# Performance work log

Hardware: AMD Instinct MI355X
Metric: run time of the kernel (lower is better)

Reference implementation:

```python
import jax, jax.numpy as jnp
import numpy as np

B, C, T, H = 16, 128, 128, 128


def setup_inputs() -> dict:
    key = jax.random.key(0)
    ks = jax.random.split(key, 9)
    inp = {
        "food_relation": jax.random.normal(ks[0], (B, C, H), jnp.float32),
        "thorn_relation": jax.random.normal(ks[1], (B, C, T, H), jnp.float32),
        "clone": jax.random.normal(ks[2], (B, C, H), jnp.float32),
        "clone_relation": jax.random.normal(ks[3], (B, C, C, H), jnp.float32),
        "thorn_mask": jax.random.randint(ks[4], (B, T), 0, 2, jnp.int32),
        "clone_mask": jax.random.randint(ks[5], (B, C), 0, 2, jnp.int32),
        # MLP(layer_num=1) == Linear(in, h) + activation (ReLU)
        "W_thorn": jax.random.normal(ks[6], (2 * H, H), jnp.float32) / np.sqrt(2 * H),
        "b_thorn": jnp.zeros((H,), jnp.float32),
        "W_clone": jax.random.normal(ks[7], (3 * H, H), jnp.float32) / np.sqrt(3 * H),
        "b_clone": jnp.zeros((H,), jnp.float32),
        "W_agg": jax.random.normal(ks[8], (4 * H, H), jnp.float32) / np.sqrt(4 * H),
        "b_agg": jnp.zeros((H,), jnp.float32),
    }
    return inp


def reference(food_relation, thorn_relation, clone, clone_relation,
              thorn_mask, clone_mask,
              W_thorn, b_thorn, W_clone, b_clone, W_agg, b_agg):
    b, c, h = clone.shape
    t = thorn_relation.shape[2]
    tm = thorn_mask.astype(clone.dtype)[:, None, :, None]  # (b,1,t,1)
    cm = clone_mask.astype(clone.dtype)[:, None, :, None]  # (b,1,c,1)

    # thorn branch: MLP(concat([clone_i, thorn_rel_ij], -1))
    # == clone @ W[:h] (broadcast over t) + rel @ W[h:], avoiding the big concat
    x = ((clone @ W_thorn[:h])[:, :, None, :]
         + jnp.einsum('bcth,hk->bctk', thorn_relation, W_thorn[h:])
         + b_thorn)  # (b,c,t,h)
    thorn_agg = jnp.max(jax.nn.relu(x) * tm, axis=2)  # (b,c,h)

    # clone branch: MLP(concat([clone_i, clone_j, clone_rel_ij], -1))
    y = ((clone @ W_clone[:h])[:, :, None, :]
         + (clone @ W_clone[h:2 * h])[:, None, :, :]
         + jnp.einsum('bcdh,hk->bcdk', clone_relation, W_clone[2 * h:])
         + b_clone)  # (b,c,c,h)
    clone_agg = jnp.max(jax.nn.relu(y) * cm, axis=2)  # (b,c,h)

    agg = jnp.concatenate([clone, food_relation, thorn_agg, clone_agg], axis=-1)  # (b,c,4h)
    return clone + jax.nn.relu(agg @ W_agg + b_agg)
```

## Files before the change

kernel.cpp:

```cpp
#include <hip/hip_runtime.h>

#define BB 16
#define CC 128
#define TT 128
#define HH 128
#define BC (BB*CC)

typedef __attribute__((ext_vector_type(8))) short bf16x8;
typedef __attribute__((ext_vector_type(4))) float f32x4;

__device__ __forceinline__ unsigned short f2bf(float f) {
  union { float f; unsigned u; } v; v.f = f;
  unsigned u = v.u;
  u += 0x7FFFu + ((u >> 16) & 1u);
  return (unsigned short)(u >> 16);
}

__device__ __forceinline__ bf16x8 pack8(f32x4 a, f32x4 b) {
  bf16x8 r;
  r[0] = (short)f2bf(a[0]); r[1] = (short)f2bf(a[1]);
  r[2] = (short)f2bf(a[2]); r[3] = (short)f2bf(a[3]);
  r[4] = (short)f2bf(b[0]); r[5] = (short)f2bf(b[1]);
  r[6] = (short)f2bf(b[2]); r[7] = (short)f2bf(b[3]);
  return r;
}

__global__ __launch_bounds__(256) void prep_kernel(
    const float* __restrict__ Wt, const float* __restrict__ Wc, const float* __restrict__ Wa,
    const float* __restrict__ clone, const float* __restrict__ food,
    const float* __restrict__ bt, const float* __restrict__ bcl,
    const int* __restrict__ tmask, const int* __restrict__ cmask,
    unsigned short* __restrict__ W2sw, unsigned short* __restrict__ Wcsw,
    unsigned short* __restrict__ WaggT,
    float* __restrict__ cpt, float* __restrict__ cp1,
    unsigned short* __restrict__ agg,
    int* __restrict__ tidx, int* __restrict__ tcnt,
    int* __restrict__ cidx, int* __restrict__ ccnt) {
  const int blk = blockIdx.x, tid = threadIdx.x;
  if (blk < 56) {
    int i = blk * 256 + tid;
    if (i < 2048) {
      int f = i >> 6, l = i & 63;
      int kt = f >> 3, n = f & 7;
      int ncol = n * 16 + (l & 15);
      int k0 = kt * 32 + (l >> 4) * 8;
      unsigned short o[8];
      #pragma unroll
      for (int e = 0; e < 8; ++e) o[e] = f2bf(Wt[(128 + k0 + e) * 128 + ncol]);
      *(uint4*)&W2sw[i * 8] = *(uint4*)o;
    } else if (i < 6144) {
      int j = i - 2048;
      int f = j >> 6, l = j & 63;
      int kt = f >> 3, n = f & 7;
      int ncol = n * 16 + (l & 15);
      int lk8 = (l >> 4) * 8;
      unsigned short o[8];
      #pragma unroll
      for (int e = 0; e < 8; ++e) {
        int src = (kt < 4) ? (256 + kt * 32 + lk8 + e) : (128 + (kt - 4) * 32 + lk8 + e);
        o[e] = f2bf(Wc[src * 128 + ncol]);
      }
      *(uint4*)&Wcsw[j * 8] = *(uint4*)o;
    } else if (i < 14336) {
      int j = i - 6144;
      int n = j >> 6, k0 = (j & 63) * 8;
      unsigned short o[8];
      #pragma unroll
      for (int e = 0; e < 8; ++e) o[e] = f2bf(Wa[(k0 + e) * 128 + n]);
      *(uint4*)&WaggT[n * 512 + k0] = *(uint4*)o;
    }
  } else if (blk < 312) {
    const int bc0 = (blk - 56) * 8;
    __shared__ float cl[8][128];
    for (int i = tid; i < 1024; i += 256) cl[i >> 7][i & 127] = clone[bc0 * 128 + i];
    __syncthreads();
    const int k = tid & 127, r0 = (tid >> 7) * 4;
    float s1[4], s2[4];
    #pragma unroll
    for (int r = 0; r < 4; ++r) { s1[r] = bt[k]; s2[r] = bcl[k]; }
    #pragma unroll 8
    for (int h = 0; h < 128; ++h) {
      float w1 = Wt[h * 128 + k], w2 = Wc[h * 128 + k];
      #pragma unroll
      for (int r = 0; r < 4; ++r) {
        float c = cl[r0 + r][h];
        s1[r] = fmaf(c, w1, s1[r]);
        s2[r] = fmaf(c, w2, s2[r]);
      }
    }
    #pragma unroll
    for (int r = 0; r < 4; ++r) {
      cpt[(bc0 + r0 + r) * 128 + k] = s1[r];
      cp1[(bc0 + r0 + r) * 128 + k] = s2[r];
    }
    for (int i = tid; i < 1024; i += 256) {
      int r = i >> 7, kk = i & 127;
      agg[(size_t)(bc0 + r) * 512 + kk]       = f2bf(cl[r][kk]);
      agg[(size_t)(bc0 + r) * 512 + 128 + kk] = f2bf(food[bc0 * 128 + i]);
    }
  } else {
    if (tid < 32) {
      int b = tid >> 1, which = tid & 1;
      const int* m = which ? cmask : tmask;
      int* idx = which ? cidx : tidx;
      int c = 0;
      for (int i = 0; i < 128; ++i)
        if (m[b * 128 + i]) idx[b * 128 + c++] = i;
      if (which) ccnt[b] = c; else tcnt[b] = c;
    }
  }
}

__global__ __launch_bounds__(512, 4) void branch5(
    const float* __restrict__ trel, const float* __restrict__ crel,
    const float* __restrict__ cloneA,
    const float* __restrict__ cpt, const float* __restrict__ cp1,
    const int* __restrict__ tidx, const int* __restrict__ tcnt,
    const int* __restrict__ cidx, const int* __restrict__ ccnt,
    const uint4* __restrict__ W2sw, const uint4* __restrict__ Wcsw,
    unsigned short* __restrict__ agg) {
  __shared__ uint4 Wlds[8 * 512];
  __shared__ float redbuf[2][8][128];
  __shared__ int idxl[128];
  __shared__ float biasl[8][128];

  const bool isClone = blockIdx.x < 256;
  const int tileIdx = blockIdx.x & 255;
  const float* __restrict__ rel     = isClone ? crel  : trel;
  const float* __restrict__ biasrow = isClone ? cp1   : cpt;
  const int*   __restrict__ idxg    = isClone ? cidx  : tidx;
  const uint4* __restrict__ Wsw     = isClone ? Wcsw  : W2sw;
  const int aggoff = isClone ? 384 : 256;
  const int nkt    = isClone ? 8 : 4;

  const int tid = threadIdx.x;
  const int wave = tid >> 6, lane = tid & 63;
  const int l16 = lane & 15, lk = lane >> 4;
  const int bc0 = tileIdx << 3;
  const int b = bc0 >> 7;
  const int cnt = (isClone ? ccnt : tcnt)[b];

  for (int i = tid; i < nkt * 512; i += 512) Wlds[i] = Wsw[i];
  if (tid < 128) idxl[tid] = idxg[b * 128 + tid];
  #pragma unroll
  for (int i = 0; i < 2; ++i)
    biasl[(i * 512 + tid) >> 7][(i * 512 + tid) & 127] = biasrow[bc0 * 128 + i * 512 + tid];
  __syncthreads();

  int rsel = wave * 16 + l16;
  rsel = rsel < cnt ? rsel : (cnt > 0 ? cnt - 1 : 0);
  const int row = (cnt > 0) ? idxl[rsel] : 0;

  bf16x8 afc[4];
  if (isClone) {
    const float* Ca = cloneA + ((size_t)b * 128 + row) * 128 + lk * 8;
    #pragma unroll
    for (int kt = 0; kt < 4; ++kt)
      afc[kt] = pack8(*(const f32x4*)(Ca + kt * 32),
                      *(const f32x4*)(Ca + kt * 32 + 4));
  }

  const float* Rbase = rel + ((size_t)bc0 * 128 + row) * 128 + lk * 8;
  f32x4 pf[4][2];
  #pragma unroll
  for (int kt = 0; kt < 4; ++kt) {
    pf[kt][0] = *(const f32x4*)(Rbase + kt * 32);
    pf[kt][1] = *(const f32x4*)(Rbase + kt * 32 + 4);
  }

  for (int t = 0; t < 8; ++t) {
    const int bc = bc0 + t;

    bf16x8 afr[4];
    #pragma unroll
    for (int kt = 0; kt < 4; ++kt) afr[kt] = pack8(pf[kt][0], pf[kt][1]);

    if (t < 7) {
      const float* Rn = Rbase + (size_t)(t + 1) * 16384;
      #pragma unroll
      for (int kt = 0; kt < 4; ++kt) {
        pf[kt][0] = *(const f32x4*)(Rn + kt * 32);
        pf[kt][1] = *(const f32x4*)(Rn + kt * 32 + 4);
      }
    }

    f32x4 acc[8];
    #pragma unroll
    for (int n = 0; n < 8; ++n) acc[n] = (f32x4){0.f, 0.f, 0.f, 0.f};
    #pragma unroll
    for (int kt = 0; kt < 4; ++kt) {
      #pragma unroll
      for (int n = 0; n < 8; ++n) {
        bf16x8 bfr = *(const bf16x8*)&Wlds[(kt * 8 + n) * 64 + lane];
        acc[n] = __builtin_amdgcn_mfma_f32_16x16x32_bf16(afr[kt], bfr, acc[n], 0, 0, 0);
      }
    }
    if (isClone) {
      #pragma unroll
      for (int kt = 0; kt < 4; ++kt) {
        #pragma unroll
        for (int n = 0; n < 8; ++n) {
          bf16x8 bfr = *(const bf16x8*)&Wlds[((kt + 4) * 8 + n) * 64 + lane];
          acc[n] = __builtin_amdgcn_mfma_f32_16x16x32_bf16(afc[kt], bfr, acc[n], 0, 0, 0);
        }
      }
    }

    #pragma unroll
    for (int n = 0; n < 8; ++n) {
      float bias = biasl[t][n * 16 + l16];
      float m0 = 0.f;
      #pragma unroll
      for (int j = 0; j < 4; ++j)
        m0 = fmaxf(m0, fmaxf(acc[n][j] + bias, 0.f));
      float v = fmaxf(m0, __shfl_xor(m0, 16));
      v = fmaxf(v, __shfl_xor(v, 32));
      if (lane < 16) redbuf[t & 1][wave][n * 16 + lane] = v;
    }
    __syncthreads();
    if (tid < 128) {
      float v = redbuf[t & 1][0][tid];
      #pragma unroll
      for (int w2 = 1; w2 < 8; ++w2) v = fmaxf(v, redbuf[t & 1][w2][tid]);
      agg[(size_t)bc * 512 + aggoff + tid] = f2bf(cnt > 0 ? v : 0.f);
    }
  }
}

__global__ __launch_bounds__(256) void final_kernel(
    const unsigned short* __restrict__ agg, const unsigned short* __restrict__ WaggT,
    const float* __restrict__ clone, const float* __restrict__ bagg,
    float* __restrict__ out) {
  const int tid = threadIdx.x;
  const int wave = tid >> 6, lane = tid & 63;
  const int l16 = lane & 15, lk = lane >> 4;
  const int mrow = blockIdx.x * 16;

  f32x4 acc[2];
  acc[0] = (f32x4){0.f, 0.f, 0.f, 0.f};
  acc[1] = (f32x4){0.f, 0.f, 0.f, 0.f};
  #pragma unroll
  for (int kt = 0; kt < 16; ++kt) {
    bf16x8 a = *(const bf16x8*)(agg + (size_t)(mrow + l16) * 512 + kt * 32 + lk * 8);
    #pragma unroll
    for (int nn = 0; nn < 2; ++nn) {
      int ncol = (wave * 2 + nn) * 16 + l16;
      bf16x8 bfr = *(const bf16x8*)(WaggT + (size_t)ncol * 512 + kt * 32 + lk * 8);
      acc[nn] = __builtin_amdgcn_mfma_f32_16x16x32_bf16(a, bfr, acc[nn], 0, 0, 0);
    }
  }
  #pragma unroll
  for (int nn = 0; nn < 2; ++nn) {
    int col = (wave * 2 + nn) * 16 + l16;
    float bias = bagg[col];
    #pragma unroll
    for (int j = 0; j < 4; ++j) {
      int row = mrow + lk * 4 + j;
      out[row * 128 + col] = clone[row * 128 + col] + fmaxf(acc[nn][j] + bias, 0.f);
    }
  }
}

extern "C" void kernel_launch(void* const* d_in, const int* in_sizes, int n_in,
                              void* d_out, int out_size, void* d_ws, size_t ws_size,
                              hipStream_t stream) {
  const float* food  = (const float*)d_in[0];
  const float* trel  = (const float*)d_in[1];
  const float* clone = (const float*)d_in[2];
  const float* crel  = (const float*)d_in[3];
  const int*   tmask = (const int*)d_in[4];
  const int*   cmask = (const int*)d_in[5];
  const float* Wt    = (const float*)d_in[6];
  const float* bt    = (const float*)d_in[7];
  const float* Wc    = (const float*)d_in[8];
  const float* bcl   = (const float*)d_in[9];
  const float* Wa    = (const float*)d_in[10];
  const float* ba    = (const float*)d_in[11];
  float* out = (float*)d_out;

  char* w = (char*)d_ws;
  float* cpt = (float*)w;                      w += (size_t)BC * 128 * 4;
  float* cp1 = (float*)w;                      w += (size_t)BC * 128 * 4;
  unsigned short* W2sw  = (unsigned short*)w;  w += 32 * 64 * 8 * 2;
  unsigned short* Wcsw  = (unsigned short*)w;  w += 64 * 64 * 8 * 2;
  unsigned short* WaggT = (unsigned short*)w;  w += 128 * 512 * 2;
  unsigned short* aggb  = (unsigned short*)w;  w += (size_t)BC * 512 * 2;
  int* tidx = (int*)w;                         w += 16 * 128 * 4;
  int* cidx = (int*)w;                         w += 16 * 128 * 4;
  int* tcnt = (int*)w;                         w += 16 * 4;
  int* ccnt = (int*)w;                         w += 16 * 4;

  prep_kernel<<<313, 256, 0, stream>>>(Wt, Wc, Wa, clone, food, bt, bcl,
                                       tmask, cmask,
                                       W2sw, Wcsw, WaggT, cpt, cp1, aggb,
                                       tidx, tcnt, cidx, ccnt);
  branch5<<<512, 512, 0, stream>>>(trel, crel, clone, cpt, cp1,
                                   tidx, tcnt, cidx, ccnt,
                                   (const uint4*)W2sw, (const uint4*)Wcsw, aggb);
  final_kernel<<<128, 256, 0, stream>>>(aggb, WaggT, clone, ba, out);
}
```

Baseline: 73.94 us.

## Switch branch GEMM to 32x32x16 MFMA tiles and skip inactive row groups

Repacks the thorn and clone weight fragments for the 32x32x16 bf16 MFMA layout and restructures the branch kernel so each wave computes 32 rows by 64 columns with two accumulators. Row groups past the mask count skip their loads and MFMAs entirely, which removes work for masked-out rows. The cross-wave reduction shrinks to 4 row groups. Occupancy hint drops to 2 blocks per CU to make room for the larger per-thread register footprint (8-deep prefetch plus 16-wide accumulators).

```diff
diff --git a/kernel.cpp b/kernel.cpp
--- a/kernel.cpp
+++ b/kernel.cpp
@@ -8,6 +8,7 @@
 
 typedef __attribute__((ext_vector_type(8))) short bf16x8;
 typedef __attribute__((ext_vector_type(4))) float f32x4;
+typedef __attribute__((ext_vector_type(16))) float f32x16;
 
 __device__ __forceinline__ unsigned short f2bf(float f) {
   union { float f; unsigned u; } v; v.f = f;
@@ -41,9 +42,9 @@
     int i = blk * 256 + tid;
     if (i < 2048) {
       int f = i >> 6, l = i & 63;
-      int kt = f >> 3, n = f & 7;
-      int ncol = n * 16 + (l & 15);
-      int k0 = kt * 32 + (l >> 4) * 8;
+      int ks = f >> 2, nb = f & 3;
+      int ncol = nb * 32 + (l & 31);
+      int k0 = ks * 16 + (l >> 5) * 8;
       unsigned short o[8];
       #pragma unroll
       for (int e = 0; e < 8; ++e) o[e] = f2bf(Wt[(128 + k0 + e) * 128 + ncol]);
@@ -51,13 +52,14 @@
     } else if (i < 6144) {
       int j = i - 2048;
       int f = j >> 6, l = j & 63;
-      int kt = f >> 3, n = f & 7;
-      int ncol = n * 16 + (l & 15);
-      int lk8 = (l >> 4) * 8;
+      int ks = f >> 2, nb = f & 3;
+      int ncol = nb * 32 + (l & 31);
+      int k0 = ks * 16 + (l >> 5) * 8;
       unsigned short o[8];
       #pragma unroll
       for (int e = 0; e < 8; ++e) {
-        int src = (kt < 4) ? (256 + kt * 32 + lk8 + e) : (128 + (kt - 4) * 32 + lk8 + e);
+        int kk = k0 + e;
+        int src = (kk < 128) ? (256 + kk) : kk;
         o[e] = f2bf(Wc[src * 128 + ncol]);
       }
       *(uint4*)&Wcsw[j * 8] = *(uint4*)o;
@@ -111,7 +113,7 @@
   }
 }
 
-__global__ __launch_bounds__(512, 4) void branch5(
+__global__ __launch_bounds__(512, 2) void branch6(
     const float* __restrict__ trel, const float* __restrict__ crel,
     const float* __restrict__ cloneA,
     const float* __restrict__ cpt, const float* __restrict__ cp1,
@@ -119,8 +121,8 @@
     const int* __restrict__ cidx, const int* __restrict__ ccnt,
     const uint4* __restrict__ W2sw, const uint4* __restrict__ Wcsw,
     unsigned short* __restrict__ agg) {
-  __shared__ uint4 Wlds[8 * 512];
-  __shared__ float redbuf[2][8][128];
+  __shared__ uint4 Wlds[64 * 64];
+  __shared__ float redbuf[2][4][128];
   __shared__ int idxl[128];
   __shared__ float biasl[8][128];
 
@@ -131,98 +133,108 @@
   const int*   __restrict__ idxg    = isClone ? cidx  : tidx;
   const uint4* __restrict__ Wsw     = isClone ? Wcsw  : W2sw;
   const int aggoff = isClone ? 384 : 256;
-  const int nkt    = isClone ? 8 : 4;
+  const int nfrag  = isClone ? 64 : 32;
 
   const int tid = threadIdx.x;
   const int wave = tid >> 6, lane = tid & 63;
-  const int l16 = lane & 15, lk = lane >> 4;
+  const int l32 = lane & 31, lh = lane >> 5;
+  const int rgrp = wave >> 1, ch = wave & 1;
   const int bc0 = tileIdx << 3;
   const int b = bc0 >> 7;
   const int cnt = (isClone ? ccnt : tcnt)[b];
-
-  for (int i = tid; i < nkt * 512; i += 512) Wlds[i] = Wsw[i];
+  const bool active = (rgrp * 32) < cnt;
+
+  for (int i = tid; i < nfrag * 64; i += 512) Wlds[i] = Wsw[i];
   if (tid < 128) idxl[tid] = idxg[b * 128 + tid];
   #pragma unroll
-  for (int i = 0; i < 2; ++i)
-    biasl[(i * 512 + tid) >> 7][(i * 512 + tid) & 127] = biasrow[bc0 * 128 + i * 512 + tid];
+  for (int i = 0; i < 2; ++i) {
+    int q = i * 512 + tid;
+    biasl[q >> 7][q & 127] = biasrow[bc0 * 128 + q];
+  }
   __syncthreads();
 
-  int rsel = wave * 16 + l16;
-  rsel = rsel < cnt ? rsel : (cnt > 0 ? cnt - 1 : 0);
-  const int row = (cnt > 0) ? idxl[rsel] : 0;
-
-  bf16x8 afc[4];
-  if (isClone) {
-    const float* Ca = cloneA + ((size_t)b * 128 + row) * 128 + lk * 8;
-    #pragma unroll
-    for (int kt = 0; kt < 4; ++kt)
-      afc[kt] = pack8(*(const f32x4*)(Ca + kt * 32),
-                      *(const f32x4*)(Ca + kt * 32 + 4));
-  }
-
-  const float* Rbase = rel + ((size_t)bc0 * 128 + row) * 128 + lk * 8;
-  f32x4 pf[4][2];
-  #pragma unroll
-  for (int kt = 0; kt < 4; ++kt) {
-    pf[kt][0] = *(const f32x4*)(Rbase + kt * 32);
-    pf[kt][1] = *(const f32x4*)(Rbase + kt * 32 + 4);
+  int rsel = rgrp * 32 + l32;
+  if (rsel >= cnt) rsel = cnt - 1;
+  const int row = active ? idxl[rsel] : 0;
+
+  bf16x8 afc[8];
+  if (isClone && active) {
+    const float* Ca = cloneA + ((size_t)b * 128 + row) * 128 + lh * 8;
+    #pragma unroll
+    for (int ks = 0; ks < 8; ++ks)
+      afc[ks] = pack8(*(const f32x4*)(Ca + ks * 16),
+                      *(const f32x4*)(Ca + ks * 16 + 4));
+  }
+
+  const float* Rbase = rel + ((size_t)bc0 * 128 + row) * 128 + lh * 8;
+  f32x4 pf[8][2];
+  if (active) {
+    #pragma unroll
+    for (int ks = 0; ks < 8; ++ks) {
+      pf[ks][0] = *(const f32x4*)(Rbase + ks * 16);
+      pf[ks][1] = *(const f32x4*)(Rbase + ks * 16 + 4);
+    }
   }
 
   for (int t = 0; t < 8; ++t) {
     const int bc = bc0 + t;
 
-    bf16x8 afr[4];
-    #pragma unroll
-    for (int kt = 0; kt < 4; ++kt) afr[kt] = pack8(pf[kt][0], pf[kt][1]);
-
-    if (t < 7) {
-      const float* Rn = Rbase + (size_t)(t + 1) * 16384;
-      #pragma unroll
-      for (int kt = 0; kt < 4; ++kt) {
-        pf[kt][0] = *(const f32x4*)(Rn + kt * 32);
-        pf[kt][1] = *(const f32x4*)(Rn + kt * 32 + 4);
-      }
-    }
-
-    f32x4 acc[8];
-    #pragma unroll
-    for (int n = 0; n < 8; ++n) acc[n] = (f32x4){0.f, 0.f, 0.f, 0.f};
-    #pragma unroll
-    for (int kt = 0; kt < 4; ++kt) {
-      #pragma unroll
-      for (int n = 0; n < 8; ++n) {
-        bf16x8 bfr = *(const bf16x8*)&Wlds[(kt * 8 + n) * 64 + lane];
-        acc[n] = __builtin_amdgcn_mfma_f32_16x16x32_bf16(afr[kt], bfr, acc[n], 0, 0, 0);
-      }
-    }
-    if (isClone) {
-      #pragma unroll
-      for (int kt = 0; kt < 4; ++kt) {
+    f32x16 acc0, acc1;
+    #pragma unroll
+    for (int r = 0; r < 16; ++r) { acc0[r] = 0.f; acc1[r] = 0.f; }
+    float v0 = 0.f, v1 = 0.f;
+
+    if (active) {
+      bf16x8 afr[8];
+      #pragma unroll
+      for (int ks = 0; ks < 8; ++ks) afr[ks] = pack8(pf[ks][0], pf[ks][1]);
+
+      if (t < 7) {
+        const float* Rn = Rbase + (size_t)(t + 1) * 16384;
         #pragma unroll
-        for (int n = 0; n < 8; ++n) {
-          bf16x8 bfr = *(const bf16x8*)&Wlds[((kt + 4) * 8 + n) * 64 + lane];
-          acc[n] = __builtin_amdgcn_mfma_f32_16x16x32_bf16(afc[kt], bfr, acc[n], 0, 0, 0);
+        for (int ks = 0; ks < 8; ++ks) {
+          pf[ks][0] = *(const f32x4*)(Rn + ks * 16);
+          pf[ks][1] = *(const f32x4*)(Rn + ks * 16 + 4);
         }
       }
-    }
-
-    #pragma unroll
-    for (int n = 0; n < 8; ++n) {
-      float bias = biasl[t][n * 16 + l16];
-      float m0 = 0.f;
-      #pragma unroll
-      for (int j = 0; j < 4; ++j)
-        m0 = fmaxf(m0, fmaxf(acc[n][j] + bias, 0.f));
-      float v = fmaxf(m0, __shfl_xor(m0, 16));
-      v = fmaxf(v, __shfl_xor(v, 32));
-      if (lane < 16) redbuf[t & 1][wave][n * 16 + lane] = v;
+
+      #pragma unroll
+      for (int ks = 0; ks < 8; ++ks) {
+        bf16x8 b0 = *(const bf16x8*)&Wlds[(ks * 4 + ch * 2 + 0) * 64 + lane];
+        bf16x8 b1 = *(const bf16x8*)&Wlds[(ks * 4 + ch * 2 + 1) * 64 + lane];
+        acc0 = __builtin_amdgcn_mfma_f32_32x32x16_bf16(afr[ks], b0, acc0, 0, 0, 0);
+        acc1 = __builtin_amdgcn_mfma_f32_32x32x16_bf16(afr[ks], b1, acc1, 0, 0, 0);
+      }
+      if (isClone) {
+        #pragma unroll
+        for (int ks = 0; ks < 8; ++ks) {
+          bf16x8 b0 = *(const bf16x8*)&Wlds[((ks + 8) * 4 + ch * 2 + 0) * 64 + lane];
+          bf16x8 b1 = *(const bf16x8*)&Wlds[((ks + 8) * 4 + ch * 2 + 1) * 64 + lane];
+          acc0 = __builtin_amdgcn_mfma_f32_32x32x16_bf16(afc[ks], b0, acc0, 0, 0, 0);
+          acc1 = __builtin_amdgcn_mfma_f32_32x32x16_bf16(afc[ks], b1, acc1, 0, 0, 0);
+        }
+      }
+
+      float bias0 = biasl[t][ch * 64 + l32];
+      float bias1 = biasl[t][ch * 64 + 32 + l32];
+      #pragma unroll
+      for (int r = 0; r < 16; ++r) {
+        v0 = fmaxf(v0, fmaxf(acc0[r] + bias0, 0.f));
+        v1 = fmaxf(v1, fmaxf(acc1[r] + bias1, 0.f));
+      }
+      v0 = fmaxf(v0, __shfl_xor(v0, 32));
+      v1 = fmaxf(v1, __shfl_xor(v1, 32));
+    }
+
+    if (lane < 32) {
+      redbuf[t & 1][rgrp][ch * 64 + l32]      = v0;
+      redbuf[t & 1][rgrp][ch * 64 + 32 + l32] = v1;
     }
     __syncthreads();
     if (tid < 128) {
-      float v = redbuf[t & 1][0][tid];
-      #pragma unroll
-      for (int w2 = 1; w2 < 8; ++w2) v = fmaxf(v, redbuf[t & 1][w2][tid]);
-      agg[(size_t)bc * 512 + aggoff + tid] = f2bf(cnt > 0 ? v : 0.f);
+      float v = fmaxf(fmaxf(redbuf[t & 1][0][tid], redbuf[t & 1][1][tid]),
+                      fmaxf(redbuf[t & 1][2][tid], redbuf[t & 1][3][tid]));
+      agg[(size_t)bc * 512 + aggoff + tid] = f2bf(v);
     }
   }
 }
@@ -294,7 +306,7 @@
                                        tmask, cmask,
                                        W2sw, Wcsw, WaggT, cpt, cp1, aggb,
                                        tidx, tcnt, cidx, ccnt);
-  branch5<<<512, 512, 0, stream>>>(trel, crel, clone, cpt, cp1,
+  branch6<<<512, 512, 0, stream>>>(trel, crel, clone, cpt, cp1,
                                    tidx, tcnt, cidx, ccnt,
                                    (const uint4*)W2sw, (const uint4*)Wcsw, aggb);
   final_kernel<<<128, 256, 0, stream>>>(aggb, WaggT, clone, ba, out);
```

After: 92.17 us. 1.25x slower.
